# Kernel optimization log

Measured on AMD Instinct MI355X. Metric: run time of the kernel, lower is better.

## Reference

```python
import jax, jax.numpy as jnp
import numpy as np

B, LI, LT, D, H, DH, E, I, IS, TOPK = 2, 1024, 256, 768, 12, 64, 8, 3072, 1536, 2


def _rms(x, s):
    # RMSNorm over last dim, eps=1e-6, learned scale s [DH]
    r = jax.lax.rsqrt(jnp.mean(x * x, axis=-1, keepdims=True) + 1e-6)
    return x * r * s


def _ln(x):
    # LayerNorm without affine (elementwise_affine=False), eps=1e-6
    m = jnp.mean(x, axis=-1, keepdims=True)
    v = jnp.mean((x - m) ** 2, axis=-1, keepdims=True)
    return (x - m) * jax.lax.rsqrt(v + 1e-6)


def _mlp(x, wg, wu, wd):
    # SwiGLU MoeMLP: down(silu(gate(x)) * up(x))
    return (jax.nn.silu(x @ wg.T) * (x @ wu.T)) @ wd.T


def _moe(x, gw, eg, eu, ed, sg, su, sd):
    # x: [T, D]. Softmax gate -> top-k (norm_topk_prob=False -> raw weights),
    # combine expert outputs weighted by routing probs, plus shared experts.
    scores = jax.nn.softmax(x @ gw.T, axis=-1)            # [T, E]
    tw, ti = jax.lax.top_k(scores, TOPK)                  # [T, K]
    T = x.shape[0]
    w = jnp.zeros((T, E), x.dtype).at[jnp.arange(T)[:, None], ti].add(tw)
    y = jnp.zeros_like(x)
    for e in range(E):  # fixed small expert count
        y = y + w[:, e:e + 1] * _mlp(x, eg[e], eu[e], ed[e])
    return y + _mlp(x, sg, su, sd)


def _mod(vec, w, b):
    # Modulation(double=True): Linear(silu(vec)) -> 6 chunks, broadcast over seq
    return jnp.split((jax.nn.silu(vec) @ w.T + b)[:, None, :], 6, axis=-1)


def _qkv(x, w, b, qs, ks):
    Bb, L, _ = x.shape
    qkv = (x @ w.T + b).reshape(Bb, L, 3, H, DH).transpose(2, 0, 3, 1, 4)  # [3,B,H,L,DH]
    q, k, v = qkv[0], qkv[1], qkv[2]
    return _rms(q, qs), _rms(k, ks), v


def _forward(img, txt, vec, imw, imb, tmw, tmb, iqkvw, iqkvb, ipw, ipb, tqkvw, tqkvb, tpw, tpb, iqs, iks, tqs, tks, igw, ieg, ieu, ied, isg, isu, isd, tgw, teg, teu, ted, tsg, tsu, tsd):
    is1, ic1, ig1, is2, ic2, ig2 = _mod(vec, imw, imb)
    ts1, tc1, tg1, ts2, tc2, tg2 = _mod(vec, tmw, tmb)
    iq, ik, iv = _qkv((1 + ic1) * _ln(img) + is1, iqkvw, iqkvb, iqs, iks)
    tq, tk, tv = _qkv((1 + tc1) * _ln(txt) + ts1, tqkvw, tqkvb, tqs, tks)
    # joint attention over concat(txt, img)
    q = jnp.concatenate([tq, iq], axis=2)
    k = jnp.concatenate([tk, ik], axis=2)
    v = jnp.concatenate([tv, iv], axis=2)
    a = jax.nn.softmax(jnp.einsum('bhqd,bhkd->bhqk', q, k) / np.float32(np.sqrt(DH)), axis=-1)
    o = jnp.einsum('bhqk,bhkd->bhqd', a, v).transpose(0, 2, 1, 3).reshape(B, LT + LI, D)
    txt_a, img_a = o[:, :LT], o[:, LT:]
    img = img + ig1 * (img_a @ ipw.T + ipb)
    txt = txt + tg1 * (txt_a @ tpw.T + tpb)
    img = img + ig2 * _moe(((1 + ic2) * _ln(img) + is2).reshape(-1, D), igw, ieg, ieu, ied, isg, isu, isd).reshape(B, LI, D)
    txt = txt + tg2 * _moe(((1 + tc2) * _ln(txt) + ts2).reshape(-1, D), tgw, teg, teu, ted, tsg, tsu, tsd).reshape(B, LT, D)
    return img, txt


def setup_inputs() -> dict:
    key = jax.random.key(0)
    ks = jax.random.split(key, 32)
    n = lambda i, sh, s=1.0: jax.random.normal(ks[i], sh, jnp.float32) * s
    W = 0.02
    return {
        'img': n(0, (B, LI, D)), 'txt': n(1, (B, LT, D)), 'vec': n(2, (B, D)),
        'imw': n(3, (6 * D, D), W), 'imb': n(4, (6 * D,), W),
        'tmw': n(5, (6 * D, D), W), 'tmb': n(6, (6 * D,), W),
        'iqkvw': n(7, (3 * D, D), W), 'iqkvb': n(8, (3 * D,), W),
        'ipw': n(9, (D, D), W), 'ipb': n(10, (D,), W),
        'tqkvw': n(11, (3 * D, D), W), 'tqkvb': n(12, (3 * D,), W),
        'tpw': n(13, (D, D), W), 'tpb': n(14, (D,), W),
        'iqs': jnp.ones((DH,), jnp.float32), 'iks': jnp.ones((DH,), jnp.float32),
        'tqs': jnp.ones((DH,), jnp.float32), 'tks': jnp.ones((DH,), jnp.float32),
        'igw': n(15, (E, D), W), 'ieg': n(16, (E, I, D), W), 'ieu': n(17, (E, I, D), W), 'ied': n(18, (E, D, I), W),
        'isg': n(19, (IS, D), W), 'isu': n(20, (IS, D), W), 'isd': n(21, (D, IS), W),
        'tgw': n(22, (E, D), W), 'teg': n(23, (E, I, D), W), 'teu': n(24, (E, I, D), W), 'ted': n(25, (E, D, I), W),
        'tsg': n(26, (IS, D), W), 'tsu': n(27, (IS, D), W), 'tsd': n(28, (D, IS), W),
    }


def reference(img, txt, vec, imw, imb, tmw, tmb, iqkvw, iqkvb, ipw, ipb, tqkvw, tqkvb, tpw, tpb, iqs, iks, tqs, tks, igw, ieg, ieu, ied, isg, isu, isd, tgw, teg, teu, ted, tsg, tsu, tsd):
    return _forward(img, txt, vec, imw, imb, tmw, tmb, iqkvw, iqkvb, ipw, ipb, tqkvw, tqkvb, tpw, tpb, iqs, iks, tqs, tks, igw, ieg, ieu, ied, isg, isu, isd, tgw, teg, teu, ted, tsg, tsu, tsd)
```

## Files before the change

### kernel.cpp

```cpp
#include <hip/hip_runtime.h>
#include <hip/hip_bf16.h>

using bf16 = __hip_bfloat16;
typedef __attribute__((ext_vector_type(4))) float f32x4;
typedef __attribute__((ext_vector_type(8))) short s16x8;

#define DEV static __device__ __forceinline__
DEV float bf2f(bf16 x){ return __bfloat162float(x); }
DEV bf16  f2bf(float x){ return __float2bfloat16(x); }
DEV float silu_(float x){ return x / (1.f + expf(-x)); }

template<bool B_F32, bool EXPERT, bool GATHER, int OUT, bool BIAS, bool FUSE>
DEV void gemm_core(
    const bf16* __restrict__ A,
    const void* __restrict__ B0a, const void* __restrict__ B0b,
    const void* __restrict__ B1a, const void* __restrict__ B1b,
    const float* __restrict__ bias, void* __restrict__ C,
    int M, int N, int K, int lda, int fuseOff,
    long a_zoff, long b_zoff, int bshift, int biasz, int nsplitB,
    int zdiv, long c_so, long c_si, int ldc,
    float alpha, int ksplit, long c_spo,
    const int* __restrict__ rowlist, const int* __restrict__ offsets,
    const int* __restrict__ counts)
{
  __shared__ __align__(16) char smem_[36864];
  bf16 (*As)[72] = (bf16(*)[72])smem_;
  bf16 (*Bs)[72] = (bf16(*)[72])(smem_ + 18432);
  float (*st)[132] = (float(*)[132])smem_;

  const int zz = blockIdx.z;
  const int z = zz / ksplit, split = zz % ksplit;
  const int m0 = blockIdx.y * 128, n0 = blockIdx.x * 128;
  int Meff = M; long rowbase = 0;
  if (EXPERT){ Meff = counts[z]; rowbase = offsets[z]; }
  if (m0 >= Meff) return;
  const bf16* Ab = A + (EXPERT ? 0 : z * a_zoff);
  const int bidx = z >> bshift;
  const long e = (long)(z & ((1 << bshift) - 1));
  const void* BL = bidx ? B1a : B0a;
  const void* BU = bidx ? B1b : B0b;
  long coff;
  if (EXPERT) coff = rowbase * (long)ldc;
  else        coff = (long)(z / zdiv) * c_so + (long)(z % zdiv) * c_si;
  coff += (long)split * c_spo;
  const float* bias_eff = BIAS ? bias + (long)bidx * biasz : nullptr;

  const int klen = K / ksplit;
  const int kbeg = split * klen;
  const int NT = klen >> 6;

  const int tid = threadIdx.x;
  const int lane = tid & 63, wid = tid >> 6;
  const int wm = wid >> 1, wn = wid & 1;

  const int rbase = tid >> 3;
  const int kc = (tid & 7) << 3;
  const bf16* ap[4]; const bf16* ap2[4];
  const bf16* bp[4]; const float* bpf[4];
  bool avalid[4], bvalid[4];
  #pragma unroll
  for (int it = 0; it < 4; it++){
    int row = rbase + 32 * it;
    long ar = 0;
    if (EXPERT){
      int i = m0 + row;
      avalid[it] = i < Meff;
      if (avalid[it]) ar = GATHER ? (long)rowlist[rowbase + i] : (rowbase + i);
    } else {
      avalid[it] = (m0 + row) < Meff;
      ar = m0 + row;
    }
    ap[it] = Ab + ar * (long)lda + kbeg + kc;
    if (FUSE) ap2[it] = ap[it] + fuseOff;
    int br = n0 + row;
    bvalid[it] = br < N;
    int brc = bvalid[it] ? br : 0;
    bool up = brc >= nsplitB;
    long brr = up ? (brc - nsplitB) : brc;
    const void* Bsel = up ? BU : BL;
    if (B_F32) bpf[it] = (const float*)Bsel + e * b_zoff + brr * K + kbeg + kc;
    else       bp[it]  = (const bf16*) Bsel + e * b_zoff + brr * K + kbeg + kc;
  }

  uint4 ra[4], ru[4], rb[4];
  float4 fb0[4], fb1[4];
  const uint4 zero4 = make_uint4(0u,0u,0u,0u);

  auto LOAD = [&](int koff){
    #pragma unroll
    for (int it = 0; it < 4; it++){
      ra[it] = avalid[it] ? *(const uint4*)(ap[it] + koff) : zero4;
      if (FUSE) ru[it] = avalid[it] ? *(const uint4*)(ap2[it] + koff) : zero4;
      if (B_F32){
        if (bvalid[it]){ fb0[it] = *(const float4*)(bpf[it] + koff);
                         fb1[it] = *(const float4*)(bpf[it] + koff + 4); }
        else { fb0[it] = make_float4(0,0,0,0); fb1[it] = make_float4(0,0,0,0); }
      } else {
        rb[it] = bvalid[it] ? *(const uint4*)(bp[it] + koff) : zero4;
      }
    }
  };
  auto STORE = [&](){
    #pragma unroll
    for (int it = 0; it < 4; it++){
      int row = rbase + 32 * it;
      uint4 av = ra[it];
      if (FUSE){
        union { bf16 h[8]; uint4 v; } g_, u_, r_;
        g_.v = ra[it]; u_.v = ru[it];
        #pragma unroll
        for (int j = 0; j < 8; j++)
          r_.h[j] = f2bf(silu_(bf2f(g_.h[j])) * bf2f(u_.h[j]));
        av = r_.v;
      }
      *(uint4*)(&As[row][kc]) = av;
      if (B_F32){
        union { bf16 h[8]; uint4 v; } u;
        u.h[0]=f2bf(fb0[it].x); u.h[1]=f2bf(fb0[it].y); u.h[2]=f2bf(fb0[it].z); u.h[3]=f2bf(fb0[it].w);
        u.h[4]=f2bf(fb1[it].x); u.h[5]=f2bf(fb1[it].y); u.h[6]=f2bf(fb1[it].z); u.h[7]=f2bf(fb1[it].w);
        *(uint4*)(&Bs[row][kc]) = u.v;
      } else {
        *(uint4*)(&Bs[row][kc]) = rb[it];
      }
    }
  };

  f32x4 acc[4][4] = {};
  LOAD(0);
  for (int t = 0; t < NT; t++){
    STORE();
    __syncthreads();
    if (t + 1 < NT) LOAD((t + 1) << 6);
    #pragma unroll
    for (int ks2 = 0; ks2 < 2; ks2++){
      const int r16 = lane & 15;
      const int kk = ks2 * 32 + ((lane >> 4) << 3);
      s16x8 af[4], bfr[4];
      #pragma unroll
      for (int mi = 0; mi < 4; mi++) af[mi]  = *(const s16x8*)(&As[wm*64 + mi*16 + r16][kk]);
      #pragma unroll
      for (int ni = 0; ni < 4; ni++) bfr[ni] = *(const s16x8*)(&Bs[wn*64 + ni*16 + r16][kk]);
      #pragma unroll
      for (int mi = 0; mi < 4; mi++)
        #pragma unroll
        for (int ni = 0; ni < 4; ni++)
          acc[mi][ni] = __builtin_amdgcn_mfma_f32_16x16x32_bf16(af[mi], bfr[ni], acc[mi][ni], 0, 0, 0);
    }
    __syncthreads();
  }

  const int er = tid >> 3;
  const int ec = (tid & 7) << 4;
  const int erg = m0 + (er & 15) + ((er & 16) ? 64 : 0);
  #pragma unroll
  for (int mi = 0; mi < 4; mi++){
    #pragma unroll
    for (int ni = 0; ni < 4; ni++){
      int lc = wn*64 + ni*16 + (lane & 15);
      float bv = 0.f;
      if (BIAS){ if (split == 0) bv = bias_eff[n0 + lc]; }
      #pragma unroll
      for (int i = 0; i < 4; i++){
        int lr = wm*16 + ((lane >> 4) << 2) + i;
        st[lr][lc] = acc[mi][ni][i] * alpha + bv;
      }
    }
    __syncthreads();
    int rg = erg + mi*16;
    int cg = n0 + ec;
    if (rg < Meff && cg < N){
      long base = coff + (long)rg * ldc + cg;
      if (OUT == 0){
        float* dst = (float*)C + base;
        #pragma unroll
        for (int q = 0; q < 4; q++)
          *(float4*)(dst + 4*q) = make_float4(st[er][ec+4*q], st[er][ec+4*q+1],
                                              st[er][ec+4*q+2], st[er][ec+4*q+3]);
      } else {
        union { bf16 h[8]; uint4 v; } o0, o1;
        #pragma unroll
        for (int j = 0; j < 8; j++){
          o0.h[j] = f2bf(st[er][ec+j]);
          o1.h[j] = f2bf(st[er][ec+8+j]);
        }
        *(uint4*)((bf16*)C + base)     = o0.v;
        *(uint4*)((bf16*)C + base + 8) = o1.v;
      }
    }
    __syncthreads();
  }
}

#define GEMM_K(NAME, BF32, EXPERT, GATHER, OUT, BIAS, FUSE)                        \
__global__ __launch_bounds__(256) void NAME(                                       \
    const bf16* A, const void* B0a, const void* B0b, const void* B1a,              \
    const void* B1b, const float* bias, void* C,                                   \
    int M, int N, int K, int lda, int fo, long az, long bz, int bshift, int biasz, \
    int nsplitB, int zdiv, long cso, long csi, int ldc, float alpha, int ks,       \
    long cspo, const int* rl, const int* ofs, const int* cnt){                     \
  gemm_core<BF32,EXPERT,GATHER,OUT,BIAS,FUSE>(A,B0a,B0b,B1a,B1b,bias,C,M,N,K,lda,  \
      fo,az,bz,bshift,biasz,nsplitB,zdiv,cso,csi,ldc,alpha,ks,cspo,rl,ofs,cnt); }

GEMM_K(k_qkv,  true ,true ,false,1,true ,false)
GEMM_K(k_qkt,  false,false,false,1,false,false)
GEMM_K(k_pv,   false,false,false,0,false,false)
GEMM_K(k_proj, true ,true ,false,0,true ,false)
GEMM_K(k_gup,  true ,true ,true ,1,false,false)
GEMM_K(k_down, true ,true ,false,0,false,true )
GEMM_K(k_sgup, true ,true ,false,1,false,false)
GEMM_K(k_sdown,true ,true ,false,0,false,true )

__global__ void init_kernel(int* cnt16, int* tabs){
  int i = threadIdx.x;
  if (i < 16) cnt16[i] = 0;
  if (i == 0){
    tabs[0]=2048; tabs[1]=512; tabs[2]=0; tabs[3]=2048;
    tabs[4]=256; tabs[5]=256; tabs[6]=1024; tabs[7]=1024;
    tabs[8]=0; tabs[9]=1280; tabs[10]=256; tabs[11]=1536;
    tabs[12]=2048; tabs[13]=512; tabs[14]=0; tabs[15]=2048;
  }
}
__global__ void tables_kernel(const int* cnt16, int* ofs16, int* cur16){
  if (threadIdx.x == 0){
    int o = 0;
    for (int e = 0; e < 8; e++){ ofs16[e] = o; o += cnt16[e]; cur16[e] = 0; }
    o = 4096;
    for (int e = 8; e < 16; e++){ ofs16[e] = o; o += cnt16[e]; cur16[e] = 0; }
  }
}

__global__ __launch_bounds__(256) void reduce_o_kernel(const float* __restrict__ Op,
    bf16* __restrict__ O, int chunk){
  int zh = blockIdx.y;
  int bh = chunk*12 + zh;
  int b = bh / 12, hh = bh % 12;
  int d = threadIdx.x & 63, rr = threadIdx.x >> 6;
  const float* base = Op + (long)zh * 1280 * 64;
  #pragma unroll
  for (int j = 0; j < 4; j++){
    int row = blockIdx.x * 16 + rr * 4 + j;
    float s = 0.f;
    #pragma unroll
    for (int sp = 0; sp < 5; sp++) s += base[(long)sp*12*1280*64 + (long)row*64 + d];
    O[((long)b*1280 + row)*768 + hh*64 + d] = f2bf(s);
  }
}

__global__ __launch_bounds__(256) void mod_kernel(const float* __restrict__ vec,
    const float* __restrict__ w, const float* __restrict__ b, float* __restrict__ out){
  int bb = blockIdx.y;
  __shared__ float sv[768];
  int tid = threadIdx.x;
  for (int i = tid; i < 768; i += 256){ float v = vec[bb*768 + i]; sv[i] = v/(1.f+expf(-v)); }
  __syncthreads();
  int w4 = tid >> 6, lane = tid & 63;
  int j0 = blockIdx.x * 8 + w4 * 2;
  for (int jj = 0; jj < 2; jj++){
    int j = j0 + jj;
    const float* wr = w + (long)j * 768;
    float p = 0.f;
    #pragma unroll
    for (int i = 0; i < 12; i++) p += sv[lane + 64*i] * wr[lane + 64*i];
    for (int o = 32; o; o >>= 1) p += __shfl_xor(p, o);
    if (lane == 0) out[bb*4608 + j] = p + b[j];
  }
}

__global__ __launch_bounds__(256) void ln_mod_kernel(const float* __restrict__ x,
    const float* __restrict__ mod, bf16* __restrict__ y, int L){
  int t = blockIdx.x; int b = t / L;
  const float* xr = x + (long)t * 768;
  __shared__ float red[256];
  int tid = threadIdx.x;
  float v[3]; float s = 0.f;
  #pragma unroll
  for (int i = 0; i < 3; i++){ v[i] = xr[tid + 256*i]; s += v[i]; }
  red[tid] = s; __syncthreads();
  for (int o = 128; o; o >>= 1){ if (tid < o) red[tid] += red[tid+o]; __syncthreads(); }
  float mean = red[0] * (1.f/768.f); __syncthreads();
  float s2 = 0.f;
  #pragma unroll
  for (int i = 0; i < 3; i++){ float d = v[i]-mean; s2 += d*d; }
  red[tid] = s2; __syncthreads();
  for (int o = 128; o; o >>= 1){ if (tid < o) red[tid] += red[tid+o]; __syncthreads(); }
  float rs = rsqrtf(red[0] * (1.f/768.f) + 1e-6f);
  const float* mb = mod + (long)b * 4608;
  #pragma unroll
  for (int i = 0; i < 3; i++){
    int d = tid + 256*i;
    y[(long)t*768 + d] = f2bf((1.f + mb[768+d]) * ((v[i]-mean)*rs) + mb[d]);
  }
}

__global__ __launch_bounds__(256) void resid_ln_mod_kernel(const float* __restrict__ x,
    const float* __restrict__ pj, int pjoff, long pjspo, const float* __restrict__ mod,
    float* __restrict__ h, bf16* __restrict__ y, float* __restrict__ yf, int L){
  int t = blockIdx.x; int b = t / L;
  const float* mb = mod + (long)b * 4608;
  const float* xr = x + (long)t * 768;
  long pr = (long)(pjoff + b*1280 + (t % L)) * 768;
  __shared__ float red[256];
  int tid = threadIdx.x;
  float v[3]; float s = 0.f;
  #pragma unroll
  for (int i = 0; i < 3; i++){
    int d = tid + 256*i;
    float pv = pj[pr + d] + pj[pjspo + pr + d];
    float hv = xr[d] + mb[2*768 + d] * pv;
    h[(long)t*768 + d] = hv;
    v[i] = hv; s += hv;
  }
  red[tid] = s; __syncthreads();
  for (int o = 128; o; o >>= 1){ if (tid < o) red[tid] += red[tid+o]; __syncthreads(); }
  float mean = red[0] * (1.f/768.f); __syncthreads();
  float s2 = 0.f;
  #pragma unroll
  for (int i = 0; i < 3; i++){ float d = v[i]-mean; s2 += d*d; }
  red[tid] = s2; __syncthreads();
  for (int o = 128; o; o >>= 1){ if (tid < o) red[tid] += red[tid+o]; __syncthreads(); }
  float rs = rsqrtf(red[0] * (1.f/768.f) + 1e-6f);
  #pragma unroll
  for (int i = 0; i < 3; i++){
    int d = tid + 256*i;
    float val = (1.f + mb[4*768+d]) * ((v[i]-mean)*rs) + mb[3*768+d];
    y[(long)t*768 + d] = f2bf(val);
    yf[(long)t*768 + d] = val;
  }
}

__global__ __launch_bounds__(256) void qkv_scatter_kernel(const bf16* __restrict__ qkv,
    const float* __restrict__ qs, const float* __restrict__ ks,
    bf16* __restrict__ Q, bf16* __restrict__ Kb, bf16* __restrict__ Vt,
    int L, int seqoff){
  __shared__ float vt[64][65];
  int bh = blockIdx.y;
  int b = bh / 12, hh = bh % 12;
  int st = blockIdx.x * 64;
  int w = threadIdx.x >> 6, lane = threadIdx.x & 63;
  float qsc = qs[lane], ksc = ks[lane];
  long qkvbase = (long)b * L * 2304;
  long outbase = (long)bh * 1280 * 64;
  #pragma unroll 4
  for (int i = 0; i < 16; i++){
    int r = w*16 + i;
    int t = st + r;
    const bf16* row = qkv + qkvbase + (long)t * 2304;
    float q = bf2f(row[hh*64 + lane]);
    float k = bf2f(row[768 + hh*64 + lane]);
    float v = bf2f(row[1536 + hh*64 + lane]);
    float q2 = q*q, k2 = k*k;
    for (int o = 32; o; o >>= 1){ q2 += __shfl_xor(q2, o); k2 += __shfl_xor(k2, o); }
    q = q * rsqrtf(q2*(1.f/64.f) + 1e-6f) * qsc;
    k = k * rsqrtf(k2*(1.f/64.f) + 1e-6f) * ksc;
    int seq = seqoff + t;
    Q [outbase + (long)seq*64 + lane] = f2bf(q);
    Kb[outbase + (long)seq*64 + lane] = f2bf(k);
    vt[r][lane] = v;
  }
  __syncthreads();
  #pragma unroll 4
  for (int i = 0; i < 16; i++){
    int d = w*16 + i;
    Vt[outbase + (long)d*1280 + seqoff + st + lane] = f2bf(vt[lane][d]);
  }
}

__global__ __launch_bounds__(256) void softmax_kernel(const bf16* __restrict__ S, bf16* __restrict__ P){
  long r = blockIdx.x;
  const bf16* sr = S + r * 1280;
  __shared__ float buf[1280];
  __shared__ float red[256];
  int tid = threadIdx.x;
  float mx = -1e30f;
  for (int i = tid; i < 1280; i += 256){ float v = bf2f(sr[i]); buf[i] = v; mx = fmaxf(mx, v); }
  red[tid] = mx; __syncthreads();
  for (int o = 128; o; o >>= 1){ if (tid < o) red[tid] = fmaxf(red[tid], red[tid+o]); __syncthreads(); }
  float m = red[0]; __syncthreads();
  float s = 0.f;
  for (int i = tid; i < 1280; i += 256){ float e = expf(buf[i] - m); buf[i] = e; s += e; }
  red[tid] = s; __syncthreads();
  for (int o = 128; o; o >>= 1){ if (tid < o) red[tid] += red[tid+o]; __syncthreads(); }
  float inv = 1.f / red[0];
  bf16* pr = P + r * 1280;
  for (int i = tid; i < 1280; i += 256) pr[i] = f2bf(buf[i] * inv);
}

__global__ __launch_bounds__(256) void router_kernel(const float* __restrict__ x2,
    const float* __restrict__ gw, float* __restrict__ tkw, int* __restrict__ tki,
    int* __restrict__ counts, int T){
  int t = blockIdx.x * 4 + (threadIdx.x >> 6);
  int lane = threadIdx.x & 63;
  if (t >= T) return;
  const float* xr = x2 + (long)t * 768;
  float xs[12];
  #pragma unroll
  for (int i = 0; i < 12; i++) xs[i] = xr[lane + 64*i];
  float sc[8];
  #pragma unroll
  for (int e = 0; e < 8; e++){
    const float* gr = gw + e * 768;
    float p = 0.f;
    #pragma unroll
    for (int i = 0; i < 12; i++) p += xs[i] * gr[lane + 64*i];
    for (int o = 32; o; o >>= 1) p += __shfl_xor(p, o);
    sc[e] = p;
  }
  if (lane == 0){
    float m = sc[0];
    for (int e = 1; e < 8; e++) m = fmaxf(m, sc[e]);
    float s = 0.f;
    for (int e = 0; e < 8; e++){ sc[e] = expf(sc[e] - m); s += sc[e]; }
    float inv = 1.f / s;
    for (int e = 0; e < 8; e++) sc[e] *= inv;
    int i0 = 0;
    for (int e = 1; e < 8; e++) if (sc[e] > sc[i0]) i0 = e;
    int i1 = -1;
    for (int e = 0; e < 8; e++){ if (e == i0) continue; if (i1 < 0 || sc[e] > sc[i1]) i1 = e; }
    tkw[t*2] = sc[i0]; tkw[t*2+1] = sc[i1];
    tki[t*2] = i0;     tki[t*2+1] = i1;
    atomicAdd(&counts[i0], 1); atomicAdd(&counts[i1], 1);
  }
}

__global__ __launch_bounds__(256) void scatter_kernel(const int* __restrict__ tki,
    const int* __restrict__ ofs16, int* __restrict__ cur16,
    int* __restrict__ rows16, int* __restrict__ tpos, int T, int tabofs, int rowadd){
  int idx = blockIdx.x * 256 + threadIdx.x;
  if (idx >= T * 2) return;
  int t = idx >> 1;
  int e = tki[idx];
  int pos = atomicAdd(&cur16[tabofs + e], 1);
  int g = ofs16[tabofs + e] + pos;
  rows16[g] = rowadd + t;
  tpos[idx] = g;
}

__global__ __launch_bounds__(256) void combine_kernel(const float* __restrict__ h,
    const float* __restrict__ mod, const float* __restrict__ tkw, const int* __restrict__ tpos,
    const float* __restrict__ ye, long espo, const float* __restrict__ ys, long sspo,
    float* __restrict__ out, int L){
  int t = blockIdx.x; int b = t / L;
  const float* g2 = mod + (long)b * 4608 + 5*768;
  float w0 = tkw[t*2], w1 = tkw[t*2+1];
  long p0 = (long)tpos[t*2] * 768, p1 = (long)tpos[t*2+1] * 768;
  for (int d = threadIdx.x; d < 768; d += 256){
    float e0 = 0.f, e1 = 0.f, sv = 0.f;
    #pragma unroll
    for (int sp = 0; sp < 4; sp++){
      e0 += ye[sp*espo + p0 + d];
      e1 += ye[sp*espo + p1 + d];
    }
    #pragma unroll
    for (int sp = 0; sp < 2; sp++) sv += ys[sp*sspo + (long)t*768 + d];
    out[(long)t*768 + d] = h[(long)t*768 + d] + g2[d] * (w0*e0 + w1*e1 + sv);
  }
}

extern "C" void kernel_launch(void* const* d_in, const int* in_sizes, int n_in,
                              void* d_out, int out_size, void* d_ws, size_t ws_size,
                              hipStream_t stream){
  (void)in_sizes; (void)n_in; (void)out_size; (void)ws_size;
  const float* fin[33];
  for (int i = 0; i < 33; i++) fin[i] = (const float*)d_in[i];
  float* out_img = (float*)d_out;
  float* out_txt = (float*)d_out + (long)2*1024*768;

  char* ws = (char*)d_ws;
  size_t off = 0;
  auto alloc = [&](size_t n)->char*{
    off = (off + 255) & ~(size_t)255;
    char* p = ws + off; off += n; return p;
  };

  float* mod_i=(float*)alloc(2*4608*4);
  float* mod_t=(float*)alloc(2*4608*4);
  float* h_i  =(float*)alloc((size_t)2048*768*4);
  float* h_t  =(float*)alloc((size_t)512*768*4);
  bf16*  x2c  =(bf16*) alloc((size_t)2560*768*2);
  float* x2fc =(float*)alloc((size_t)2560*768*4);
  float* tkw_i=(float*)alloc(2048*2*4);
  int*   tki_i=(int*)  alloc(2048*2*4);
  float* tkw_t=(float*)alloc(512*2*4);
  int*   tki_t=(int*)  alloc(512*2*4);
  int* cnt16=(int*)alloc(16*4);
  int* ofs16=(int*)alloc(16*4);
  int* cur16=(int*)alloc(16*4);
  int* rows16=(int*)alloc(5120*4);
  int* tpos_i=(int*)alloc(4096*4);
  int* tpos_t=(int*)alloc(1024*4);
  int* tabs=(int*)alloc(64*4);
  float* qb_ws=(float*)alloc(2*2304*4);
  float* pb_ws=(float*)alloc(2*768*4);

  size_t arena = (off + 255) & ~(size_t)255;
  off = arena;
  bf16* Qb=(bf16*)alloc((size_t)24*1280*64*2);
  bf16* Kb=(bf16*)alloc((size_t)24*1280*64*2);
  bf16* Vt=(bf16*)alloc((size_t)24*1280*64*2);
  bf16* O =(bf16*)alloc((size_t)2*1280*768*2);
  float* pjc=(float*)alloc((size_t)2*2560*768*4);
  size_t sub = (off + 255) & ~(size_t)255;
  bf16* xmc=(bf16*)alloc((size_t)2560*768*2);
  bf16* qrc=(bf16*)alloc((size_t)2560*2304*2);
  off = sub;
  bf16* S=(bf16*)alloc((size_t)12*1280*1280*2);
  float* Opart=(float*)alloc((size_t)5*12*1280*64*4);
  off = arena;
  bf16*  h1gu =(bf16*) alloc((size_t)5120*6144*2);
  float* ye   =(float*)alloc((size_t)4*5120*768*4);
  bf16*  h1sgu=(bf16*) alloc((size_t)2560*3072*2);
  float* ys   =(float*)alloc((size_t)2*2560*768*4);

  hipMemcpyAsync(qb_ws,      fin[8],  2304*4, hipMemcpyDeviceToDevice, stream);
  hipMemcpyAsync(qb_ws+2304, fin[12], 2304*4, hipMemcpyDeviceToDevice, stream);
  hipMemcpyAsync(pb_ws,      fin[14], 768*4,  hipMemcpyDeviceToDevice, stream);
  hipMemcpyAsync(pb_ws+768,  fin[10], 768*4,  hipMemcpyDeviceToDevice, stream);

  init_kernel<<<1, 64, 0, stream>>>(cnt16, tabs);
  mod_kernel<<<dim3(576,2), 256, 0, stream>>>(fin[2], fin[3], fin[4], mod_i);
  mod_kernel<<<dim3(576,2), 256, 0, stream>>>(fin[2], fin[5], fin[6], mod_t);
  ln_mod_kernel<<<2048, 256, 0, stream>>>(fin[0], mod_i, xmc, 1024);
  ln_mod_kernel<<<512,  256, 0, stream>>>(fin[1], mod_t, xmc + (long)2048*768, 256);

  k_qkv<<<dim3(18,16,2), 256, 0, stream>>>(xmc, fin[7], fin[7], fin[11], fin[11],
      qb_ws, qrc, 0, 2304, 768, 768, 0, 0, 0, 0, 2304, 2304,
      1, 0, 0, 2304, 1.f, 1, 0, nullptr, tabs+2, tabs+0);
  qkv_scatter_kernel<<<dim3(16,24), 256, 0, stream>>>(qrc, fin[15], fin[16], Qb, Kb, Vt, 1024, 256);
  qkv_scatter_kernel<<<dim3(4,24),  256, 0, stream>>>(qrc + (long)2048*2304, fin[17], fin[18], Qb, Kb, Vt, 256, 0);

  for (int ch = 0; ch < 2; ch++){
    const bf16* Qc = Qb + (size_t)ch * 12 * 1280 * 64;
    const bf16* Kc = Kb + (size_t)ch * 12 * 1280 * 64;
    const bf16* Vc = Vt + (size_t)ch * 12 * 1280 * 64;
    k_qkt<<<dim3(10,10,12), 256, 0, stream>>>(Qc, Kc, Kc, Kc, Kc, nullptr, S,
        1280, 1280, 64, 64, 0, (long)1280*64, (long)1280*64, 30, 0, 1280,
        1, (long)1280*1280, 0, 1280, 0.125f, 1, 0, nullptr, nullptr, nullptr);
    softmax_kernel<<<12*1280, 256, 0, stream>>>(S, S);
    k_pv<<<dim3(1,10,60), 256, 0, stream>>>(S, Vc, Vc, Vc, Vc, nullptr, Opart,
        1280, 64, 1280, 1280, 0, (long)1280*1280, (long)64*1280, 30, 0, 64,
        1, (long)1280*64, 0, 64, 1.f, 5, (long)12*1280*64, nullptr, nullptr, nullptr);
    reduce_o_kernel<<<dim3(80,12), 256, 0, stream>>>(Opart, O, ch);
  }

  k_proj<<<dim3(6,8,8), 256, 0, stream>>>(O, fin[13], fin[13], fin[9], fin[9],
      pb_ws, pjc, 0, 768, 768, 768, 0, 0, 0, 1, 768, 768,
      1, 0, 0, 768, 1.f, 2, (long)2560*768, nullptr, tabs+8, tabs+4);
  resid_ln_mod_kernel<<<2048, 256, 0, stream>>>(fin[0], pjc, 256, (long)2560*768,
      mod_i, h_i, x2c, x2fc, 1024);
  resid_ln_mod_kernel<<<512, 256, 0, stream>>>(fin[1], pjc, 0, (long)2560*768,
      mod_t, h_t, x2c + (long)2048*768, x2fc + (long)2048*768, 256);

  router_kernel<<<512, 256, 0, stream>>>(x2fc, fin[19], tkw_i, tki_i, cnt16, 2048);
  router_kernel<<<128, 256, 0, stream>>>(x2fc + (long)2048*768, fin[26], tkw_t, tki_t, cnt16+8, 512);
  tables_kernel<<<1, 1, 0, stream>>>(cnt16, ofs16, cur16);
  scatter_kernel<<<16, 256, 0, stream>>>(tki_i, ofs16, cur16, rows16, tpos_i, 2048, 0, 0);
  scatter_kernel<<<4,  256, 0, stream>>>(tki_t, ofs16, cur16, rows16, tpos_t, 512, 8, 2048);

  k_gup<<<dim3(48,16,16), 256, 0, stream>>>(x2c, fin[20], fin[21], fin[27], fin[28],
      nullptr, h1gu, 0, 6144, 768, 768, 0, 0, (long)3072*768, 3, 0, 3072,
      1, 0, 0, 6144, 1.f, 1, 0, rows16, ofs16, cnt16);
  k_down<<<dim3(6,16,64), 256, 0, stream>>>(h1gu, fin[22], fin[22], fin[29], fin[29],
      nullptr, ye, 0, 768, 3072, 6144, 3072, 0, (long)768*3072, 3, 0, 768,
      1, 0, 0, 768, 1.f, 4, (long)5120*768, nullptr, ofs16, cnt16);
  k_sgup<<<dim3(24,16,2), 256, 0, stream>>>(x2c, fin[23], fin[24], fin[30], fin[31],
      nullptr, h1sgu, 0, 3072, 768, 768, 0, 0, 0, 0, 0, 1536,
      1, 0, 0, 3072, 1.f, 1, 0, nullptr, tabs+14, tabs+12);
  k_sdown<<<dim3(6,16,4), 256, 0, stream>>>(h1sgu, fin[25], fin[25], fin[32], fin[32],
      nullptr, ys, 0, 768, 1536, 3072, 1536, 0, 0, 0, 0, 768,
      1, 0, 0, 768, 1.f, 2, (long)2560*768, nullptr, tabs+14, tabs+12);

  combine_kernel<<<2048, 256, 0, stream>>>(h_i, mod_i, tkw_i, tpos_i,
      ye, (long)5120*768, ys, (long)2560*768, out_img, 1024);
  combine_kernel<<<512, 256, 0, stream>>>(h_t, mod_t, tkw_t, tpos_t,
      ye, (long)5120*768, ys + (long)2048*768, (long)2560*768, out_txt, 256);
}
```

Before: 1.162 ms.

## Fuse SwiGLU into gate/up GEMM epilogue, loop expert M tiles in-block

Gate and up weight rows are interleaved (PAIRB), so each output tile holds matching gate/up column pairs. The epilogue then writes silu(g)*u directly as a half-width bf16 intermediate, instead of storing a full 6144-wide g|u buffer and fusing in the down GEMM's A-load. Expert GEMMs now loop over M tiles inside one block (MLOOP) rather than launching a fixed 16 y-blocks that mostly exit early. The expert down projection uses 8 K-splits, and the combine step sums 8 partials. This halves intermediate traffic and removes SiLU work from the down-GEMM inner loop, at the cost of serialising M tiles per block and adding more split-K partial reductions.

```diff
diff --git a/kernel.cpp b/kernel.cpp
--- a/kernel.cpp
+++ b/kernel.cpp
@@ -10,13 +10,13 @@
 DEV bf16  f2bf(float x){ return __float2bfloat16(x); }
 DEV float silu_(float x){ return x / (1.f + expf(-x)); }
 
-template<bool B_F32, bool EXPERT, bool GATHER, int OUT, bool BIAS, bool FUSE>
+template<bool B_F32, bool EXPERT, bool GATHER, int OUT, bool BIAS, bool PAIRB, bool MLOOP>
 DEV void gemm_core(
     const bf16* __restrict__ A,
     const void* __restrict__ B0a, const void* __restrict__ B0b,
     const void* __restrict__ B1a, const void* __restrict__ B1b,
     const float* __restrict__ bias, void* __restrict__ C,
-    int M, int N, int K, int lda, int fuseOff,
+    int M, int N, int K, int lda,
     long a_zoff, long b_zoff, int bshift, int biasz, int nsplitB,
     int zdiv, long c_so, long c_si, int ldc,
     float alpha, int ksplit, long c_spo,
@@ -30,9 +30,10 @@
 
   const int zz = blockIdx.z;
   const int z = zz / ksplit, split = zz % ksplit;
-  const int m0 = blockIdx.y * 128, n0 = blockIdx.x * 128;
+  const int n0 = blockIdx.x * 128;
   int Meff = M; long rowbase = 0;
   if (EXPERT){ Meff = counts[z]; rowbase = offsets[z]; }
+  int m0 = MLOOP ? 0 : blockIdx.y * 128;
   if (m0 >= Meff) return;
   const bf16* Ab = A + (EXPERT ? 0 : z * a_zoff);
   const int bidx = z >> bshift;
@@ -52,163 +53,171 @@
   const int tid = threadIdx.x;
   const int lane = tid & 63, wid = tid >> 6;
   const int wm = wid >> 1, wn = wid & 1;
-
   const int rbase = tid >> 3;
   const int kc = (tid & 7) << 3;
-  const bf16* ap[4]; const bf16* ap2[4];
+
   const bf16* bp[4]; const float* bpf[4];
-  bool avalid[4], bvalid[4];
+  bool bvalid[4];
   #pragma unroll
   for (int it = 0; it < 4; it++){
-    int row = rbase + 32 * it;
-    long ar = 0;
-    if (EXPERT){
-      int i = m0 + row;
-      avalid[it] = i < Meff;
-      if (avalid[it]) ar = GATHER ? (long)rowlist[rowbase + i] : (rowbase + i);
-    } else {
-      avalid[it] = (m0 + row) < Meff;
-      ar = m0 + row;
-    }
-    ap[it] = Ab + ar * (long)lda + kbeg + kc;
-    if (FUSE) ap2[it] = ap[it] + fuseOff;
-    int br = n0 + row;
+    int br = n0 + rbase + 32 * it;
     bvalid[it] = br < N;
     int brc = bvalid[it] ? br : 0;
-    bool up = brc >= nsplitB;
-    long brr = up ? (brc - nsplitB) : brc;
-    const void* Bsel = up ? BU : BL;
+    const void* Bsel; long brr;
+    if (PAIRB){ Bsel = (brc & 1) ? BU : BL; brr = brc >> 1; }
+    else { bool up = brc >= nsplitB; Bsel = up ? BU : BL; brr = up ? (brc - nsplitB) : brc; }
     if (B_F32) bpf[it] = (const float*)Bsel + e * b_zoff + brr * K + kbeg + kc;
     else       bp[it]  = (const bf16*) Bsel + e * b_zoff + brr * K + kbeg + kc;
   }
 
-  uint4 ra[4], ru[4], rb[4];
-  float4 fb0[4], fb1[4];
   const uint4 zero4 = make_uint4(0u,0u,0u,0u);
-
-  auto LOAD = [&](int koff){
-    #pragma unroll
-    for (int it = 0; it < 4; it++){
-      ra[it] = avalid[it] ? *(const uint4*)(ap[it] + koff) : zero4;
-      if (FUSE) ru[it] = avalid[it] ? *(const uint4*)(ap2[it] + koff) : zero4;
-      if (B_F32){
-        if (bvalid[it]){ fb0[it] = *(const float4*)(bpf[it] + koff);
-                         fb1[it] = *(const float4*)(bpf[it] + koff + 4); }
-        else { fb0[it] = make_float4(0,0,0,0); fb1[it] = make_float4(0,0,0,0); }
-      } else {
-        rb[it] = bvalid[it] ? *(const uint4*)(bp[it] + koff) : zero4;
-      }
-    }
-  };
-  auto STORE = [&](){
+  const int er = tid >> 3;
+  const int ec = (tid & 7) << 4;
+
+  do {
+    const bf16* ap[4];
+    bool avalid[4];
     #pragma unroll
     for (int it = 0; it < 4; it++){
       int row = rbase + 32 * it;
-      uint4 av = ra[it];
-      if (FUSE){
-        union { bf16 h[8]; uint4 v; } g_, u_, r_;
-        g_.v = ra[it]; u_.v = ru[it];
+      long ar = 0;
+      if (EXPERT){
+        int i = m0 + row;
+        avalid[it] = i < Meff;
+        if (avalid[it]) ar = GATHER ? (long)rowlist[rowbase + i] : (rowbase + i);
+      } else {
+        avalid[it] = (m0 + row) < Meff;
+        ar = m0 + row;
+      }
+      ap[it] = Ab + ar * (long)lda + kbeg + kc;
+    }
+
+    uint4 ra[4], rb[4];
+    float4 fb0[4], fb1[4];
+    auto LOAD = [&](int koff){
+      #pragma unroll
+      for (int it = 0; it < 4; it++){
+        ra[it] = avalid[it] ? *(const uint4*)(ap[it] + koff) : zero4;
+        if (B_F32){
+          if (bvalid[it]){ fb0[it] = *(const float4*)(bpf[it] + koff);
+                           fb1[it] = *(const float4*)(bpf[it] + koff + 4); }
+          else { fb0[it] = make_float4(0,0,0,0); fb1[it] = make_float4(0,0,0,0); }
+        } else {
+          rb[it] = bvalid[it] ? *(const uint4*)(bp[it] + koff) : zero4;
+        }
+      }
+    };
+    auto STORE = [&](){
+      #pragma unroll
+      for (int it = 0; it < 4; it++){
+        int row = rbase + 32 * it;
+        *(uint4*)(&As[row][kc]) = ra[it];
+        if (B_F32){
+          union { bf16 h[8]; uint4 v; } u;
+          u.h[0]=f2bf(fb0[it].x); u.h[1]=f2bf(fb0[it].y); u.h[2]=f2bf(fb0[it].z); u.h[3]=f2bf(fb0[it].w);
+          u.h[4]=f2bf(fb1[it].x); u.h[5]=f2bf(fb1[it].y); u.h[6]=f2bf(fb1[it].z); u.h[7]=f2bf(fb1[it].w);
+          *(uint4*)(&Bs[row][kc]) = u.v;
+        } else {
+          *(uint4*)(&Bs[row][kc]) = rb[it];
+        }
+      }
+    };
+
+    f32x4 acc[4][4] = {};
+    LOAD(0);
+    for (int t = 0; t < NT; t++){
+      STORE();
+      __syncthreads();
+      if (t + 1 < NT) LOAD((t + 1) << 6);
+      #pragma unroll
+      for (int ks2 = 0; ks2 < 2; ks2++){
+        const int r16 = lane & 15;
+        const int kk = ks2 * 32 + ((lane >> 4) << 3);
+        s16x8 af[4], bfr[4];
         #pragma unroll
-        for (int j = 0; j < 8; j++)
-          r_.h[j] = f2bf(silu_(bf2f(g_.h[j])) * bf2f(u_.h[j]));
-        av = r_.v;
+        for (int mi = 0; mi < 4; mi++) af[mi]  = *(const s16x8*)(&As[wm*64 + mi*16 + r16][kk]);
+        #pragma unroll
+        for (int ni = 0; ni < 4; ni++) bfr[ni] = *(const s16x8*)(&Bs[wn*64 + ni*16 + r16][kk]);
+        #pragma unroll
+        for (int mi = 0; mi < 4; mi++)
+          #pragma unroll
+          for (int ni = 0; ni < 4; ni++)
+            acc[mi][ni] = __builtin_amdgcn_mfma_f32_16x16x32_bf16(af[mi], bfr[ni], acc[mi][ni], 0, 0, 0);
       }
-      *(uint4*)(&As[row][kc]) = av;
-      if (B_F32){
-        union { bf16 h[8]; uint4 v; } u;
-        u.h[0]=f2bf(fb0[it].x); u.h[1]=f2bf(fb0[it].y); u.h[2]=f2bf(fb0[it].z); u.h[3]=f2bf(fb0[it].w);
-        u.h[4]=f2bf(fb1[it].x); u.h[5]=f2bf(fb1[it].y); u.h[6]=f2bf(fb1[it].z); u.h[7]=f2bf(fb1[it].w);
-        *(uint4*)(&Bs[row][kc]) = u.v;
-      } else {
-        *(uint4*)(&Bs[row][kc]) = rb[it];
+      __syncthreads();
+    }
+
+    const int erg = m0 + (er & 15) + ((er & 16) ? 64 : 0);
+    #pragma unroll
+    for (int mi = 0; mi < 4; mi++){
+      #pragma unroll
+      for (int ni = 0; ni < 4; ni++){
+        int lc = wn*64 + ni*16 + (lane & 15);
+        float bv = 0.f;
+        if (BIAS){ if (split == 0) bv = bias_eff[n0 + lc]; }
+        #pragma unroll
+        for (int i = 0; i < 4; i++){
+          int lr = wm*16 + ((lane >> 4) << 2) + i;
+          st[lr][lc] = acc[mi][ni][i] * alpha + bv;
+        }
       }
+      __syncthreads();
+      int rg = erg + mi*16;
+      if (rg < Meff){
+        if (OUT == 3){
+          long base = coff + (long)rg * ldc + ((n0 + ec) >> 1);
+          union { bf16 h[8]; uint4 v; } o;
+          #pragma unroll
+          for (int j = 0; j < 8; j++)
+            o.h[j] = f2bf(silu_(st[er][ec + 2*j]) * st[er][ec + 2*j + 1]);
+          *(uint4*)((bf16*)C + base) = o.v;
+        } else {
+          int cg = n0 + ec;
+          if (cg < N){
+            long base = coff + (long)rg * ldc + cg;
+            if (OUT == 0){
+              float* dst = (float*)C + base;
+              #pragma unroll
+              for (int q = 0; q < 4; q++)
+                *(float4*)(dst + 4*q) = make_float4(st[er][ec+4*q], st[er][ec+4*q+1],
+                                                    st[er][ec+4*q+2], st[er][ec+4*q+3]);
+            } else {
+              union { bf16 h[8]; uint4 v; } o0, o1;
+              #pragma unroll
+              for (int j = 0; j < 8; j++){
+                o0.h[j] = f2bf(st[er][ec+j]);
+                o1.h[j] = f2bf(st[er][ec+8+j]);
+              }
+              *(uint4*)((bf16*)C + base)     = o0.v;
+              *(uint4*)((bf16*)C + base + 8) = o1.v;
+            }
+          }
+        }
+      }
+      __syncthreads();
     }
-  };
-
-  f32x4 acc[4][4] = {};
-  LOAD(0);
-  for (int t = 0; t < NT; t++){
-    STORE();
-    __syncthreads();
-    if (t + 1 < NT) LOAD((t + 1) << 6);
-    #pragma unroll
-    for (int ks2 = 0; ks2 < 2; ks2++){
-      const int r16 = lane & 15;
-      const int kk = ks2 * 32 + ((lane >> 4) << 3);
-      s16x8 af[4], bfr[4];
-      #pragma unroll
-      for (int mi = 0; mi < 4; mi++) af[mi]  = *(const s16x8*)(&As[wm*64 + mi*16 + r16][kk]);
-      #pragma unroll
-      for (int ni = 0; ni < 4; ni++) bfr[ni] = *(const s16x8*)(&Bs[wn*64 + ni*16 + r16][kk]);
-      #pragma unroll
-      for (int mi = 0; mi < 4; mi++)
-        #pragma unroll
-        for (int ni = 0; ni < 4; ni++)
-          acc[mi][ni] = __builtin_amdgcn_mfma_f32_16x16x32_bf16(af[mi], bfr[ni], acc[mi][ni], 0, 0, 0);
-    }
-    __syncthreads();
-  }
-
-  const int er = tid >> 3;
-  const int ec = (tid & 7) << 4;
-  const int erg = m0 + (er & 15) + ((er & 16) ? 64 : 0);
-  #pragma unroll
-  for (int mi = 0; mi < 4; mi++){
-    #pragma unroll
-    for (int ni = 0; ni < 4; ni++){
-      int lc = wn*64 + ni*16 + (lane & 15);
-      float bv = 0.f;
-      if (BIAS){ if (split == 0) bv = bias_eff[n0 + lc]; }
-      #pragma unroll
-      for (int i = 0; i < 4; i++){
-        int lr = wm*16 + ((lane >> 4) << 2) + i;
-        st[lr][lc] = acc[mi][ni][i] * alpha + bv;
-      }
-    }
-    __syncthreads();
-    int rg = erg + mi*16;
-    int cg = n0 + ec;
-    if (rg < Meff && cg < N){
-      long base = coff + (long)rg * ldc + cg;
-      if (OUT == 0){
-        float* dst = (float*)C + base;
-        #pragma unroll
-        for (int q = 0; q < 4; q++)
-          *(float4*)(dst + 4*q) = make_float4(st[er][ec+4*q], st[er][ec+4*q+1],
-                                              st[er][ec+4*q+2], st[er][ec+4*q+3]);
-      } else {
-        union { bf16 h[8]; uint4 v; } o0, o1;
-        #pragma unroll
-        for (int j = 0; j < 8; j++){
-          o0.h[j] = f2bf(st[er][ec+j]);
-          o1.h[j] = f2bf(st[er][ec+8+j]);
-        }
-        *(uint4*)((bf16*)C + base)     = o0.v;
-        *(uint4*)((bf16*)C + base + 8) = o1.v;
-      }
-    }
-    __syncthreads();
-  }
-}
-
-#define GEMM_K(NAME, BF32, EXPERT, GATHER, OUT, BIAS, FUSE)                        \
+    m0 += 128;
+  } while (MLOOP && m0 < Meff);
+}
+
+#define GEMM_K(NAME, BF32, EXPERT, GATHER, OUT, BIAS, PAIRB, MLOOP)                \
 __global__ __launch_bounds__(256) void NAME(                                       \
     const bf16* A, const void* B0a, const void* B0b, const void* B1a,              \
     const void* B1b, const float* bias, void* C,                                   \
-    int M, int N, int K, int lda, int fo, long az, long bz, int bshift, int biasz, \
+    int M, int N, int K, int lda, long az, long bz, int bshift, int biasz,         \
     int nsplitB, int zdiv, long cso, long csi, int ldc, float alpha, int ks,       \
     long cspo, const int* rl, const int* ofs, const int* cnt){                     \
-  gemm_core<BF32,EXPERT,GATHER,OUT,BIAS,FUSE>(A,B0a,B0b,B1a,B1b,bias,C,M,N,K,lda,  \
-      fo,az,bz,bshift,biasz,nsplitB,zdiv,cso,csi,ldc,alpha,ks,cspo,rl,ofs,cnt); }
-
-GEMM_K(k_qkv,  true ,true ,false,1,true ,false)
-GEMM_K(k_qkt,  false,false,false,1,false,false)
-GEMM_K(k_pv,   false,false,false,0,false,false)
-GEMM_K(k_proj, true ,true ,false,0,true ,false)
-GEMM_K(k_gup,  true ,true ,true ,1,false,false)
-GEMM_K(k_down, true ,true ,false,0,false,true )
-GEMM_K(k_sgup, true ,true ,false,1,false,false)
-GEMM_K(k_sdown,true ,true ,false,0,false,true )
+  gemm_core<BF32,EXPERT,GATHER,OUT,BIAS,PAIRB,MLOOP>(A,B0a,B0b,B1a,B1b,bias,C,M,N, \
+      K,lda,az,bz,bshift,biasz,nsplitB,zdiv,cso,csi,ldc,alpha,ks,cspo,rl,ofs,cnt); }
+
+GEMM_K(k_qkv,  true ,true ,false,1,true ,false,false)
+GEMM_K(k_qkt,  false,false,false,1,false,false,false)
+GEMM_K(k_pv,   false,false,false,0,false,false,false)
+GEMM_K(k_proj, true ,true ,false,0,true ,false,false)
+GEMM_K(k_gup,  true ,true ,true ,3,false,true ,true )
+GEMM_K(k_down, true ,true ,false,0,false,false,true )
+GEMM_K(k_sgup, true ,true ,false,3,false,true ,false)
+GEMM_K(k_sdown,true ,true ,false,0,false,false,false)
 
 __global__ void init_kernel(int* cnt16, int* tabs){
   int i = threadIdx.x;
@@ -446,7 +455,7 @@
   for (int d = threadIdx.x; d < 768; d += 256){
     float e0 = 0.f, e1 = 0.f, sv = 0.f;
     #pragma unroll
-    for (int sp = 0; sp < 4; sp++){
+    for (int sp = 0; sp < 8; sp++){
       e0 += ye[sp*espo + p0 + d];
       e1 += ye[sp*espo + p1 + d];
     }
@@ -506,10 +515,10 @@
   bf16* S=(bf16*)alloc((size_t)12*1280*1280*2);
   float* Opart=(float*)alloc((size_t)5*12*1280*64*4);
   off = arena;
-  bf16*  h1gu =(bf16*) alloc((size_t)5120*6144*2);
-  float* ye   =(float*)alloc((size_t)4*5120*768*4);
-  bf16*  h1sgu=(bf16*) alloc((size_t)2560*3072*2);
-  float* ys   =(float*)alloc((size_t)2*2560*768*4);
+  bf16*  h1 =(bf16*) alloc((size_t)5120*3072*2);
+  float* ye =(float*)alloc((size_t)8*5120*768*4);
+  bf16*  h1s=(bf16*) alloc((size_t)2560*1536*2);
+  float* ys =(float*)alloc((size_t)2*2560*768*4);
 
   hipMemcpyAsync(qb_ws,      fin[8],  2304*4, hipMemcpyDeviceToDevice, stream);
   hipMemcpyAsync(qb_ws+2304, fin[12], 2304*4, hipMemcpyDeviceToDevice, stream);
@@ -523,7 +532,7 @@
   ln_mod_kernel<<<512,  256, 0, stream>>>(fin[1], mod_t, xmc + (long)2048*768, 256);
 
   k_qkv<<<dim3(18,16,2), 256, 0, stream>>>(xmc, fin[7], fin[7], fin[11], fin[11],
-      qb_ws, qrc, 0, 2304, 768, 768, 0, 0, 0, 0, 2304, 2304,
+      qb_ws, qrc, 0, 2304, 768, 768, 0, 0, 0, 2304, 2304,
       1, 0, 0, 2304, 1.f, 1, 0, nullptr, tabs+2, tabs+0);
   qkv_scatter_kernel<<<dim3(16,24), 256, 0, stream>>>(qrc, fin[15], fin[16], Qb, Kb, Vt, 1024, 256);
   qkv_scatter_kernel<<<dim3(4,24),  256, 0, stream>>>(qrc + (long)2048*2304, fin[17], fin[18], Qb, Kb, Vt, 256, 0);
@@ -533,17 +542,17 @@
     const bf16* Kc = Kb + (size_t)ch * 12 * 1280 * 64;
     const bf16* Vc = Vt + (size_t)ch * 12 * 1280 * 64;
     k_qkt<<<dim3(10,10,12), 256, 0, stream>>>(Qc, Kc, Kc, Kc, Kc, nullptr, S,
-        1280, 1280, 64, 64, 0, (long)1280*64, (long)1280*64, 30, 0, 1280,
+        1280, 1280, 64, 64, (long)1280*64, (long)1280*64, 30, 0, 1280,
         1, (long)1280*1280, 0, 1280, 0.125f, 1, 0, nullptr, nullptr, nullptr);
     softmax_kernel<<<12*1280, 256, 0, stream>>>(S, S);
     k_pv<<<dim3(1,10,60), 256, 0, stream>>>(S, Vc, Vc, Vc, Vc, nullptr, Opart,
-        1280, 64, 1280, 1280, 0, (long)1280*1280, (long)64*1280, 30, 0, 64,
+        1280, 64, 1280, 1280, (long)1280*1280, (long)64*1280, 30, 0, 64,
         1, (long)1280*64, 0, 64, 1.f, 5, (long)12*1280*64, nullptr, nullptr, nullptr);
     reduce_o_kernel<<<dim3(80,12), 256, 0, stream>>>(Opart, O, ch);
   }
 
   k_proj<<<dim3(6,8,8), 256, 0, stream>>>(O, fin[13], fin[13], fin[9], fin[9],
-      pb_ws, pjc, 0, 768, 768, 768, 0, 0, 0, 1, 768, 768,
+      pb_ws, pjc, 0, 768, 768, 768, 0, 0, 1, 768, 768,
       1, 0, 0, 768, 1.f, 2, (long)2560*768, nullptr, tabs+8, tabs+4);
   resid_ln_mod_kernel<<<2048, 256, 0, stream>>>(fin[0], pjc, 256, (long)2560*768,
       mod_i, h_i, x2c, x2fc, 1024);
@@ -556,17 +565,17 @@
   scatter_kernel<<<16, 256, 0, stream>>>(tki_i, ofs16, cur16, rows16, tpos_i, 2048, 0, 0);
   scatter_kernel<<<4,  256, 0, stream>>>(tki_t, ofs16, cur16, rows16, tpos_t, 512, 8, 2048);
 
-  k_gup<<<dim3(48,16,16), 256, 0, stream>>>(x2c, fin[20], fin[21], fin[27], fin[28],
-      nullptr, h1gu, 0, 6144, 768, 768, 0, 0, (long)3072*768, 3, 0, 3072,
-      1, 0, 0, 6144, 1.f, 1, 0, rows16, ofs16, cnt16);
-  k_down<<<dim3(6,16,64), 256, 0, stream>>>(h1gu, fin[22], fin[22], fin[29], fin[29],
-      nullptr, ye, 0, 768, 3072, 6144, 3072, 0, (long)768*3072, 3, 0, 768,
-      1, 0, 0, 768, 1.f, 4, (long)5120*768, nullptr, ofs16, cnt16);
+  k_gup<<<dim3(48,1,16), 256, 0, stream>>>(x2c, fin[20], fin[21], fin[27], fin[28],
+      nullptr, h1, 0, 6144, 768, 768, 0, (long)3072*768, 3, 0, 0,
+      1, 0, 0, 3072, 1.f, 1, 0, rows16, ofs16, cnt16);
+  k_down<<<dim3(6,1,128), 256, 0, stream>>>(h1, fin[22], fin[22], fin[29], fin[29],
+      nullptr, ye, 0, 768, 3072, 3072, 0, (long)768*3072, 3, 0, 768,
+      1, 0, 0, 768, 1.f, 8, (long)5120*768, nullptr, ofs16, cnt16);
   k_sgup<<<dim3(24,16,2), 256, 0, stream>>>(x2c, fin[23], fin[24], fin[30], fin[31],
-      nullptr, h1sgu, 0, 3072, 768, 768, 0, 0, 0, 0, 0, 1536,
-      1, 0, 0, 3072, 1.f, 1, 0, nullptr, tabs+14, tabs+12);
-  k_sdown<<<dim3(6,16,4), 256, 0, stream>>>(h1sgu, fin[25], fin[25], fin[32], fin[32],
-      nullptr, ys, 0, 768, 1536, 3072, 1536, 0, 0, 0, 0, 768,
+      nullptr, h1s, 0, 3072, 768, 768, 0, 0, 0, 0, 0,
+      1, 0, 0, 1536, 1.f, 1, 0, nullptr, tabs+14, tabs+12);
+  k_sdown<<<dim3(6,16,4), 256, 0, stream>>>(h1s, fin[25], fin[25], fin[32], fin[32],
+      nullptr, ys, 0, 768, 1536, 1536, 0, 0, 0, 0, 768,
       1, 0, 0, 768, 1.f, 2, (long)2560*768, nullptr, tabs+14, tabs+12);
 
   combine_kernel<<<2048, 256, 0, stream>>>(h_i, mod_i, tkw_i, tpos_i,
```

After: 1.125 ms. 1.03x faster.
